# Kernel optimization log

Measured on AMD Instinct MI355X. Metric: run time of the kernel, lower is better.

The kernel has to match this reference:

```python
import jax, jax.numpy as jnp
import numpy as np

B, H, L, D = 8, 8, 512, 512
NV = 8            # n_vars
TOP_P = 0.5
ALPHA = 0.5
EPS = 1e-10


def setup_inputs() -> dict:
    key = jax.random.key(0)
    ks = jax.random.split(key, 8)
    dh = D // H
    x = jax.random.normal(ks[0], (B, L, D), jnp.float32)
    # structural masks [L, 3, L]: S (same position across vars), T (same var block), ST (rest)
    N = L // NV
    idx = jnp.arange(L)
    kk = idx[:, None]
    S = ((idx[None, :] % N == kk % N) & (idx[None, :] != kk)).astype(jnp.float32)
    T = ((idx[None, :] >= (kk // N) * N) & (idx[None, :] < (kk // N) * N + N)).astype(jnp.float32)
    ST = 1.0 - S - T
    masks = jnp.stack([S, T, ST], axis=1)  # [L, 3, L]
    s = 0.05
    W1 = jax.random.normal(ks[1], (dh, dh), jnp.float32) * s
    b1 = jnp.zeros((dh,), jnp.float32)
    W2 = jax.random.normal(ks[2], (dh, dh), jnp.float32) * s
    b2 = jnp.zeros((dh,), jnp.float32)
    Wg = jax.random.normal(ks[3], (3, L), jnp.float32) * s   # gate: Linear(L, 3, bias=False)
    Wp = jax.random.normal(ks[4], (D, D), jnp.float32) * s   # GCN proj
    bp = jnp.zeros((D,), jnp.float32)
    return {"x": x, "masks": masks, "W1": W1, "b1": b1, "W2": W2, "b2": b2,
            "Wg": Wg, "Wp": Wp, "bp": bp}


def _forward(x, masks, W1, b1, W2, b2, Wg, Wp, bp):
    Bb, Ll, Dd = x.shape
    dh = Dd // H
    xh = x.reshape(Bb, Ll, H, dh).transpose(0, 2, 1, 3)          # [B,H,L,dh]
    q = xh @ W1.T + b1
    k = xh @ W2.T + b2
    adj = jax.nn.gelu(jnp.einsum('bhid,bhjd->bhij', q, k), approximate=False)  # [B,H,L,L]
    # mask_topk: zero out the k smallest entries per row (largest=False)
    ksm = int(ALPHA * Ll)
    thr = jnp.sort(adj, axis=-1)[..., ksm - 1:ksm]               # k-th smallest value
    adj = adj * (adj > thr).astype(adj.dtype)
    # ---- mask_moe (eval mode: clean logits) ----
    xf = adj.reshape(Bb * H, Ll, Ll)
    logits = jax.nn.softmax(xf @ Wg.T, axis=-1)                  # [BH,L,3]
    loss_dyn = -(logits * jnp.log(logits + EPS)).sum(axis=1).mean()
    order = jnp.argsort(-logits, axis=-1)                        # descending
    sorted_probs = jnp.take_along_axis(logits, order, axis=-1)
    cum = jnp.cumsum(sorted_probs, axis=-1)
    m = cum > TOP_P
    thr_idx = jnp.argmax(m.astype(jnp.int32), axis=-1)           # first expert crossing top_p
    thr_mask = jax.nn.one_hot(thr_idx, 3, dtype=jnp.bool_)
    m = m & (~thr_mask)                                          # True = dropped sorted slot
    selected = (~m).astype(jnp.float32)                          # [BH,L,3] over sorted slots
    # scatter selection back to original expert order
    top_p_mask = jnp.einsum('blj,blje->ble', selected, jax.nn.one_hot(order, 3, dtype=jnp.float32))
    sp = jnp.where(m, 0.0, sorted_probs)
    imp = sp.sum(axis=0)                                         # [L,3]
    loss_imp = jnp.var(imp, ddof=1) / (jnp.mean(imp) ** 2 + EPS)
    loss = loss_imp + 0.1 * loss_dyn
    gates = top_p_mask.reshape(Bb, H, Ll, 3)
    mask = jnp.einsum('bhli,lid->bhld', gates, masks) + jnp.eye(Ll, dtype=jnp.float32)[None, None]
    adj = adj * mask
    # ---- softmax + GCN ----
    adj = jax.nn.softmax(adj, axis=-1)
    adj = adj / jnp.clip(jnp.abs(adj).sum(axis=-1, keepdims=True), 1e-12)  # F.normalize p=1
    xp = (x @ Wp.T + bp).reshape(Bb, Ll, H, dh)                  # [B,L,H,dh]
    out = jnp.einsum('bhij,bjhd->bihd', adj, xp).reshape(Bb, Ll, Dd)
    return out, loss


def reference(x, masks, W1, b1, W2, b2, Wg, Wp, bp):
    return _forward(x, masks, W1, b1, W2, b2, Wg, Wp, bp)
```

## Files before the change

### kernel.cpp

```cpp
#include <hip/hip_runtime.h>
#include <hip/hip_bf16.h>
#include <math.h>

static constexpr int kB = 8;
static constexpr int kH = 8;
static constexpr int kL = 512;
static constexpr int kD = 512;
static constexpr int kDH = 64;
static constexpr int kBH = 64;
static constexpr int kROWS = kBH * kL;

typedef short bf16x8 __attribute__((ext_vector_type(8)));
typedef float f32x4 __attribute__((ext_vector_type(4)));

__device__ __forceinline__ ushort f2bf(float f) {
    unsigned u = __float_as_uint(f);
    unsigned r = u + 0x7fffu + ((u >> 16) & 1u);
    return (ushort)(r >> 16);
}
__device__ __forceinline__ float bf2f(ushort h) {
    return __uint_as_float((unsigned)h << 16);
}
__device__ __forceinline__ unsigned mapf(float f) {
    unsigned u = __float_as_uint(f);
    return (u & 0x80000000u) ? ~u : (u | 0x80000000u);
}
__device__ __forceinline__ float unmapf(unsigned u) {
    return (u & 0x80000000u) ? __uint_as_float(u ^ 0x80000000u)
                             : __uint_as_float(~u);
}

__device__ __forceinline__ float gelu_fast(float v) {
    float z = v * 0.70710678118654752440f;
    float az = fabsf(z);
    float t = 1.0f / (1.0f + 0.3275911f * az);
    float ex = __expf(-az * az);
    float poly = t * (0.254829592f + t * (-0.284496736f + t * (1.421413741f +
                 t * (-1.453152027f + t * 1.061405429f))));
    float erfv = 1.0f - poly * ex;
    erfv = (z < 0.0f) ? -erfv : erfv;
    return 0.5f * v * (1.0f + erfv);
}

__global__ __launch_bounds__(256) void k_qk(const float* __restrict__ x,
        const float* __restrict__ W1, const float* __restrict__ b1,
        const float* __restrict__ W2, const float* __restrict__ b2,
        ushort* __restrict__ qh, ushort* __restrict__ ql,
        ushort* __restrict__ kh, ushort* __restrict__ kl) {
    int blk = blockIdx.x;
    int b = blk >> 6, h = (blk >> 3) & 7, lt = blk & 7;
    __shared__ float xt[64][68];
    __shared__ float w1t[64][68];
    __shared__ float w2t[64][68];
    int tid = threadIdx.x;
    #pragma unroll
    for (int r = 0; r < 16; ++r) {
        int e = tid + r * 256;
        int rr = e >> 6, cc = e & 63;
        xt[rr][cc]  = x[(b * kL + lt * 64 + rr) * kD + h * kDH + cc];
        w1t[rr][cc] = W1[rr * 64 + cc];
        w2t[rr][cc] = W2[rr * 64 + cc];
    }
    __syncthreads();
    int ty = tid >> 4, tx = tid & 15;
    float aq[4][4] = {}, ak[4][4] = {};
    #pragma unroll 2
    for (int c = 0; c < 64; c += 4) {
        float4 av[4], wq[4], wk[4];
        #pragma unroll
        for (int a = 0; a < 4; ++a) av[a] = *(const float4*)&xt[ty * 4 + a][c];
        #pragma unroll
        for (int j = 0; j < 4; ++j) {
            wq[j] = *(const float4*)&w1t[tx + 16 * j][c];
            wk[j] = *(const float4*)&w2t[tx + 16 * j][c];
        }
        #pragma unroll
        for (int a = 0; a < 4; ++a)
            #pragma unroll
            for (int j = 0; j < 4; ++j) {
                aq[a][j] = fmaf(av[a].x, wq[j].x, aq[a][j]);
                aq[a][j] = fmaf(av[a].y, wq[j].y, aq[a][j]);
                aq[a][j] = fmaf(av[a].z, wq[j].z, aq[a][j]);
                aq[a][j] = fmaf(av[a].w, wq[j].w, aq[a][j]);
                ak[a][j] = fmaf(av[a].x, wk[j].x, ak[a][j]);
                ak[a][j] = fmaf(av[a].y, wk[j].y, ak[a][j]);
                ak[a][j] = fmaf(av[a].z, wk[j].z, ak[a][j]);
                ak[a][j] = fmaf(av[a].w, wk[j].w, ak[a][j]);
            }
    }
    #pragma unroll
    for (int a = 0; a < 4; ++a)
        #pragma unroll
        for (int j = 0; j < 4; ++j) {
            int row = lt * 64 + ty * 4 + a;
            int col = tx + 16 * j;
            int o = ((b * kH + h) * kL + row) * kDH + col;
            float qv = aq[a][j] + b1[col];
            float kv = ak[a][j] + b2[col];
            ushort qhh = f2bf(qv), khh = f2bf(kv);
            qh[o] = qhh; ql[o] = f2bf(qv - bf2f(qhh));
            kh[o] = khh; kl[o] = f2bf(kv - bf2f(khh));
        }
}

__global__ __launch_bounds__(256) void k_adj(const ushort* __restrict__ qh,
        const ushort* __restrict__ ql, const ushort* __restrict__ kh,
        const ushort* __restrict__ kl, float* __restrict__ adj) {
    int blk = blockIdx.x;
    int bh = blk >> 6;
    int it = (blk >> 3) & 7, jt = blk & 7;
    __shared__ ushort ah[64][72], al[64][72];
    __shared__ ushort bh_[64][72], bl[64][72];
    int tid = threadIdx.x;
    int r = tid >> 2, s = tid & 3;
    size_t aoff = (size_t)(bh * kL + it * 64 + r) * kDH + s * 16;
    size_t boff = (size_t)(bh * kL + jt * 64 + r) * kDH + s * 16;
    *(int4*)&ah[r][s * 16]  = *(const int4*)&qh[aoff];
    *(int4*)&ah[r][s * 16 + 8]  = *(const int4*)&qh[aoff + 8];
    *(int4*)&al[r][s * 16]  = *(const int4*)&ql[aoff];
    *(int4*)&al[r][s * 16 + 8]  = *(const int4*)&ql[aoff + 8];
    *(int4*)&bh_[r][s * 16] = *(const int4*)&kh[boff];
    *(int4*)&bh_[r][s * 16 + 8] = *(const int4*)&kh[boff + 8];
    *(int4*)&bl[r][s * 16]  = *(const int4*)&kl[boff];
    *(int4*)&bl[r][s * 16 + 8]  = *(const int4*)&kl[boff + 8];
    __syncthreads();
    int lane = tid & 63, wave = tid >> 6;
    int wm = wave >> 1, wn = wave & 1;
    int am = wm * 32 + (lane & 15);
    int bn = wn * 32 + (lane & 15);
    int coff = (lane >> 4) * 8;
    f32x4 acc[2][2] = {};
    #pragma unroll
    for (int kk = 0; kk < 2; ++kk) {
        bf16x8 afh[2], afl[2], bfh[2], bfl[2];
        #pragma unroll
        for (int fm = 0; fm < 2; ++fm) {
            afh[fm] = *(const bf16x8*)&ah[am + fm * 16][kk * 32 + coff];
            afl[fm] = *(const bf16x8*)&al[am + fm * 16][kk * 32 + coff];
        }
        #pragma unroll
        for (int fn = 0; fn < 2; ++fn) {
            bfh[fn] = *(const bf16x8*)&bh_[bn + fn * 16][kk * 32 + coff];
            bfl[fn] = *(const bf16x8*)&bl[bn + fn * 16][kk * 32 + coff];
        }
        #pragma unroll
        for (int fm = 0; fm < 2; ++fm)
            #pragma unroll
            for (int fn = 0; fn < 2; ++fn) {
                acc[fm][fn] = __builtin_amdgcn_mfma_f32_16x16x32_bf16(
                    afh[fm], bfh[fn], acc[fm][fn], 0, 0, 0);
                acc[fm][fn] = __builtin_amdgcn_mfma_f32_16x16x32_bf16(
                    afh[fm], bfl[fn], acc[fm][fn], 0, 0, 0);
                acc[fm][fn] = __builtin_amdgcn_mfma_f32_16x16x32_bf16(
                    afl[fm], bfh[fn], acc[fm][fn], 0, 0, 0);
            }
    }
    int mrow = it * 64 + wm * 32 + (lane >> 4) * 4;
    int ncol = jt * 64 + wn * 32 + (lane & 15);
    #pragma unroll
    for (int fm = 0; fm < 2; ++fm)
        #pragma unroll
        for (int fn = 0; fn < 2; ++fn)
            #pragma unroll
            for (int rr = 0; rr < 4; ++rr)
                adj[((size_t)bh * kL + mrow + fm * 16 + rr) * kL + ncol + fn * 16] =
                    gelu_fast(acc[fm][fn][rr]);
}

__global__ __launch_bounds__(256) void k_select(const float* __restrict__ adj,
        const float* __restrict__ Wg,
        ushort* __restrict__ adjb,
        float* __restrict__ spbuf, float* __restrict__ entbuf) {
    int tid = threadIdx.x;
    int wave = tid >> 6, lane = tid & 63;
    int row = blockIdx.x * 4 + wave;
    int i = row & (kL - 1);
    const float* arow = adj + (size_t)row * kL;
    int j0 = lane * 8;

    float v[8];
    {
        float4 a0 = *(const float4*)&arow[j0];
        float4 a1 = *(const float4*)&arow[j0 + 4];
        v[0] = a0.x; v[1] = a0.y; v[2] = a0.z; v[3] = a0.w;
        v[4] = a1.x; v[5] = a1.y; v[6] = a1.z; v[7] = a1.w;
    }
    unsigned key[8];
    #pragma unroll
    for (int t = 0; t < 8; ++t) key[t] = mapf(v[t]);

    unsigned prefix = 0;
    int cbp = 0, cin = 512;
    int bit = 31;
    int mode = 0;
    while (bit >= 1) {
        unsigned qsz = 1u << (bit - 1);
        unsigned q1 = prefix + qsz;
        unsigned q2 = prefix + 2u * qsz;
        unsigned q3 = prefix + 3u * qsz;
        int c1 = 0, c2 = 0, c3 = 0;
        #pragma unroll
        for (int t = 0; t < 8; ++t) {
            c1 += (int)__popcll(__ballot(key[t] < q1));
            c2 += (int)__popcll(__ballot(key[t] < q2));
            c3 += (int)__popcll(__ballot(key[t] < q3));
        }
        if (255 < c1)      { cin = c1 - cbp; }
        else if (255 < c2) { cin = c2 - c1;  prefix = q1; cbp = c1; }
        else if (255 < c3) { cin = c3 - c2;  prefix = q2; cbp = c2; }
        else               { cin = cin - (c3 - cbp); prefix = q3; cbp = c3; }
        bit -= 2;
        int loc = 255 - cbp;
        if (cin == 1)        { mode = 2; break; }
        if (loc == 0)        { mode = 1; break; }
        if (loc == cin - 1)  { mode = 2; break; }
    }
    float thr;
    if (mode == 0) {
        thr = unmapf(prefix);
    } else {
        unsigned width = 1u << (bit + 1);
        unsigned acc = (mode == 1) ? 0xFFFFFFFFu : 0u;
        #pragma unroll
        for (int t = 0; t < 8; ++t) {
            unsigned d = key[t] - prefix;
            bool mem = d < width;
            if (mode == 1) acc = (mem && key[t] < acc) ? key[t] : acc;
            else           acc = (mem && key[t] > acc) ? key[t] : acc;
        }
        if (mode == 1) {
            #pragma unroll
            for (int off = 1; off < 64; off <<= 1)
                acc = min(acc, (unsigned)__shfl_xor((int)acc, off));
        } else {
            #pragma unroll
            for (int off = 1; off < 64; off <<= 1)
                acc = max(acc, (unsigned)__shfl_xor((int)acc, off));
        }
        thr = unmapf(acc);
    }

    union { float4 f4[2]; float f[8]; } wg0, wg1, wg2;
    wg0.f4[0] = *(const float4*)&Wg[j0];          wg0.f4[1] = *(const float4*)&Wg[j0 + 4];
    wg1.f4[0] = *(const float4*)&Wg[kL + j0];     wg1.f4[1] = *(const float4*)&Wg[kL + j0 + 4];
    wg2.f4[0] = *(const float4*)&Wg[2 * kL + j0]; wg2.f4[1] = *(const float4*)&Wg[2 * kL + j0 + 4];
    float l0 = 0.f, l1 = 0.f, l2 = 0.f;
    #pragma unroll
    for (int t = 0; t < 8; ++t) {
        float nv = (v[t] > thr) ? v[t] : 0.0f;
        v[t] = nv;
        l0 = fmaf(nv, wg0.f[t], l0);
        l1 = fmaf(nv, wg1.f[t], l1);
        l2 = fmaf(nv, wg2.f[t], l2);
    }
    #pragma unroll
    for (int off = 1; off < 64; off <<= 1) {
        l0 += __shfl_xor(l0, off);
        l1 += __shfl_xor(l1, off);
        l2 += __shfl_xor(l2, off);
    }
    float m = fmaxf(l0, fmaxf(l1, l2));
    float e0 = __expf(l0 - m), e1 = __expf(l1 - m), e2 = __expf(l2 - m);
    float s = e0 + e1 + e2;
    float p[3] = {e0 / s, e1 / s, e2 / s};
    int o0, o1, o2;
    if (p[0] >= p[1] && p[0] >= p[2]) o0 = 0;
    else if (p[1] >= p[2]) o0 = 1;
    else o0 = 2;
    int r0 = (o0 == 0) ? 1 : 0;
    int r1 = (o0 == 2) ? 1 : 2;
    if (p[r0] >= p[r1]) { o1 = r0; o2 = r1; } else { o1 = r1; o2 = r0; }
    float sp0 = p[o0], sp1 = p[o1], sp2 = p[o2];
    float c0 = sp0, c1 = sp0 + sp1, c2 = c1 + sp2;
    bool m0 = c0 > 0.5f, m1 = c1 > 0.5f, m2 = c2 > 0.5f;
    int ti = m0 ? 0 : (m1 ? 1 : 2);
    bool mm0 = m0 && (ti != 0);
    bool mm1 = m1 && (ti != 1);
    bool mm2 = m2 && (ti != 2);
    float g[3] = {0.f, 0.f, 0.f};
    g[o0] = mm0 ? 0.f : 1.f;
    g[o1] = mm1 ? 0.f : 1.f;
    g[o2] = mm2 ? 0.f : 1.f;
    if (lane == 0) {
        spbuf[row * 3 + 0] = mm0 ? 0.f : sp0;
        spbuf[row * 3 + 1] = mm1 ? 0.f : sp1;
        spbuf[row * 3 + 2] = mm2 ? 0.f : sp2;
        entbuf[row] = p[0] * __logf(p[0] + 1e-10f) +
                      p[1] * __logf(p[1] + 1e-10f) +
                      p[2] * __logf(p[2] + 1e-10f);
    }

    int i6 = i >> 6, i63 = i & 63;
    bool inb = ((lane >> 3) == i6);
    float sel1 = inb ? (g[1] + 1.0f) : g[0];
    float sel0 = inb ? g[1] : g[2];
    int lane8 = (lane & 7) * 8;
    float e[8], ls = 0.f;
    #pragma unroll
    for (int t = 0; t < 8; ++t) {
        bool ing = (lane8 + t) == i63;
        float av = v[t] * (ing ? sel1 : sel0);
        e[t] = __expf(av);
        ls += e[t];
    }
    #pragma unroll
    for (int off = 1; off < 64; off <<= 1) ls += __shfl_xor(ls, off);
    float inv = 1.0f / ls;
    union { ushort u[8]; int4 vv; } pk;
    #pragma unroll
    for (int t = 0; t < 8; ++t) pk.u[t] = f2bf(e[t] * inv);
    *(int4*)&adjb[(size_t)row * kL + j0] = pk.vv;
}

__global__ __launch_bounds__(256) void k_xp(const float* __restrict__ x,
        const float* __restrict__ Wp, const float* __restrict__ bp,
        ushort* __restrict__ xpbT) {
    int it = blockIdx.x >> 3, jt = blockIdx.x & 7;
    __shared__ ushort xbs[64][72];
    __shared__ ushort wbs[64][72];
    int tid = threadIdx.x;
    int r = tid >> 2, s = tid & 3;
    int lane = tid & 63, wave = tid >> 6;
    int wm = wave >> 1, wn = wave & 1;
    int am = wm * 32 + (lane & 15);
    int bn = wn * 32 + (lane & 15);
    int coff = (lane >> 4) * 8;
    f32x4 acc[2][2] = {};
    const float* xsrc = x + (size_t)(it * 64 + r) * kD + s * 16;
    const float* wsrc = Wp + (size_t)(jt * 64 + r) * kD + s * 16;
    for (int kt = 0; kt < 8; ++kt) {
        union { ushort u[16]; int4 v[2]; } px, pw;
        #pragma unroll
        for (int c4 = 0; c4 < 4; ++c4) {
            float4 fx = *(const float4*)(xsrc + kt * 64 + c4 * 4);
            float4 fw = *(const float4*)(wsrc + kt * 64 + c4 * 4);
            px.u[c4 * 4 + 0] = f2bf(fx.x); px.u[c4 * 4 + 1] = f2bf(fx.y);
            px.u[c4 * 4 + 2] = f2bf(fx.z); px.u[c4 * 4 + 3] = f2bf(fx.w);
            pw.u[c4 * 4 + 0] = f2bf(fw.x); pw.u[c4 * 4 + 1] = f2bf(fw.y);
            pw.u[c4 * 4 + 2] = f2bf(fw.z); pw.u[c4 * 4 + 3] = f2bf(fw.w);
        }
        __syncthreads();
        *(int4*)&xbs[r][s * 16] = px.v[0];
        *(int4*)&xbs[r][s * 16 + 8] = px.v[1];
        *(int4*)&wbs[r][s * 16] = pw.v[0];
        *(int4*)&wbs[r][s * 16 + 8] = pw.v[1];
        __syncthreads();
        #pragma unroll
        for (int kk = 0; kk < 2; ++kk) {
            bf16x8 af[2], bf[2];
            #pragma unroll
            for (int fm = 0; fm < 2; ++fm)
                af[fm] = *(const bf16x8*)&xbs[am + fm * 16][kk * 32 + coff];
            #pragma unroll
            for (int fn = 0; fn < 2; ++fn)
                bf[fn] = *(const bf16x8*)&wbs[bn + fn * 16][kk * 32 + coff];
            #pragma unroll
            for (int fm = 0; fm < 2; ++fm)
                #pragma unroll
                for (int fn = 0; fn < 2; ++fn)
                    acc[fm][fn] = __builtin_amdgcn_mfma_f32_16x16x32_bf16(
                        af[fm], bf[fn], acc[fm][fn], 0, 0, 0);
        }
    }
    #pragma unroll
    for (int fn = 0; fn < 2; ++fn) {
        int dcol = jt * 64 + wn * 32 + (lane & 15) + fn * 16;
        float bpv = bp[dcol];
        #pragma unroll
        for (int fm = 0; fm < 2; ++fm) {
            int l0 = it * 64 + wm * 32 + fm * 16 + (lane >> 4) * 4;
            union { ushort u[4]; uint2 v; } pk;
            #pragma unroll
            for (int rr = 0; rr < 4; ++rr)
                pk.u[rr] = f2bf(acc[fm][fn][rr] + bpv);
            *(uint2*)&xpbT[(size_t)dcol * (size_t)(kB * kL) + l0] = pk.v;
        }
    }
}

__global__ __launch_bounds__(256) void k_out(const ushort* __restrict__ adjb,
        const ushort* __restrict__ xpbT, float* __restrict__ out) {
    int blk = blockIdx.x;
    int bh = blk >> 3, it = blk & 7;
    int b = bh >> 3, h = bh & 7;
    __shared__ ushort as_[64][72];
    __shared__ ushort bs_[64][72];
    int tid = threadIdx.x;
    int lane = tid & 63, wave = tid >> 6;
    int wm = wave >> 1, wn = wave & 1;
    int r = tid >> 2, s = tid & 3;
    const ushort* aG = adjb + ((size_t)(bh * kL + it * 64 + r)) * kL + s * 16;
    const ushort* bG = xpbT + ((size_t)(h * kDH + r)) * (size_t)(kB * kL) + b * kL + s * 16;
    f32x4 acc[2][2] = {};
    int am = wm * 32 + (lane & 15);
    int bn = wn * 32 + (lane & 15);
    int coff = (lane >> 4) * 8;
    for (int kt = 0; kt < 8; ++kt) {
        int4 a0 = *(const int4*)(aG + kt * 64);
        int4 a1 = *(const int4*)(aG + kt * 64 + 8);
        int4 b0 = *(const int4*)(bG + kt * 64);
        int4 b1 = *(const int4*)(bG + kt * 64 + 8);
        __syncthreads();
        *(int4*)&as_[r][s * 16] = a0;
        *(int4*)&as_[r][s * 16 + 8] = a1;
        *(int4*)&bs_[r][s * 16] = b0;
        *(int4*)&bs_[r][s * 16 + 8] = b1;
        __syncthreads();
        #pragma unroll
        for (int kk = 0; kk < 2; ++kk) {
            bf16x8 af[2], bf[2];
            #pragma unroll
            for (int fm = 0; fm < 2; ++fm)
                af[fm] = *(const bf16x8*)&as_[am + fm * 16][kk * 32 + coff];
            #pragma unroll
            for (int fn = 0; fn < 2; ++fn)
                bf[fn] = *(const bf16x8*)&bs_[bn + fn * 16][kk * 32 + coff];
            #pragma unroll
            for (int fm = 0; fm < 2; ++fm)
                #pragma unroll
                for (int fn = 0; fn < 2; ++fn)
                    acc[fm][fn] = __builtin_amdgcn_mfma_f32_16x16x32_bf16(
                        af[fm], bf[fn], acc[fm][fn], 0, 0, 0);
        }
    }
    int mrow = it * 64 + wm * 32 + (lane >> 4) * 4;
    int ncol = h * kDH + wn * 32 + (lane & 15);
    #pragma unroll
    for (int fm = 0; fm < 2; ++fm)
        #pragma unroll
        for (int fn = 0; fn < 2; ++fn)
            #pragma unroll
            for (int rr = 0; rr < 4; ++rr)
                out[((size_t)b * kL + mrow + fm * 16 + rr) * kD + ncol + fn * 16] =
                    acc[fm][fn][rr];
}

__global__ __launch_bounds__(256) void k_loss1(const float* __restrict__ spbuf,
        const float* __restrict__ entbuf, float* __restrict__ imps_buf,
        float* __restrict__ entpart) {
    int tid = threadIdx.x;
    int blk = blockIdx.x;
    if (blk < 6) {
        int idx = blk * 256 + tid;
        float s = 0.f;
        for (int bh = 0; bh < kBH; ++bh)
            s += spbuf[bh * (kL * 3) + idx];
        imps_buf[idx] = s;
    } else {
        int eb = blk - 6;
        const float* src = entbuf + eb * 1024 + tid * 4;
        float4 v4 = *(const float4*)src;
        float s = v4.x + v4.y + v4.z + v4.w;
        __shared__ float red[256];
        red[tid] = s;
        __syncthreads();
        for (int st = 128; st > 0; st >>= 1) {
            if (tid < st) red[tid] += red[tid + st];
            __syncthreads();
        }
        if (tid == 0) entpart[eb] = red[0];
    }
}

__global__ __launch_bounds__(256) void k_loss2(const float* __restrict__ imps_buf,
        const float* __restrict__ entpart, float* __restrict__ out_loss) {
    __shared__ float red[256];
    int tid = threadIdx.x;
    float im[6];
    #pragma unroll
    for (int t = 0; t < 6; ++t) im[t] = imps_buf[t * 256 + tid];
    float ms = im[0] + im[1] + im[2] + im[3] + im[4] + im[5];
    red[tid] = ms;
    __syncthreads();
    for (int st = 128; st > 0; st >>= 1) {
        if (tid < st) red[tid] += red[tid + st];
        __syncthreads();
    }
    float mean = red[0] / (float)(kL * 3);
    __syncthreads();
    float vs = 0.f;
    #pragma unroll
    for (int t = 0; t < 6; ++t) { float d = im[t] - mean; vs = fmaf(d, d, vs); }
    red[tid] = vs;
    __syncthreads();
    for (int st = 128; st > 0; st >>= 1) {
        if (tid < st) red[tid] += red[tid + st];
        __syncthreads();
    }
    float var = red[0] / (float)(kL * 3 - 1);
    __syncthreads();
    red[tid] = (tid < 32) ? entpart[tid] : 0.f;
    __syncthreads();
    for (int st = 128; st > 0; st >>= 1) {
        if (tid < st) red[tid] += red[tid + st];
        __syncthreads();
    }
    if (tid == 0) {
        float loss_imp = var / (mean * mean + 1e-10f);
        float loss_dyn = -red[0] / (float)(kBH * 3);
        out_loss[0] = loss_imp + 0.1f * loss_dyn;
    }
}

extern "C" void kernel_launch(void* const* d_in, const int* in_sizes, int n_in,
                              void* d_out, int out_size, void* d_ws, size_t ws_size,
                              hipStream_t stream) {
    const float* x     = (const float*)d_in[0];
    const float* W1    = (const float*)d_in[2];
    const float* b1    = (const float*)d_in[3];
    const float* W2    = (const float*)d_in[4];
    const float* b2    = (const float*)d_in[5];
    const float* Wg    = (const float*)d_in[6];
    const float* Wp    = (const float*)d_in[7];
    const float* bp    = (const float*)d_in[8];
    float* out = (float*)d_out;
    float* ws  = (float*)d_ws;

    float*  adj    = ws;
    ushort* qh     = (ushort*)(ws + 16777216);
    ushort* ql     = (ushort*)(ws + 17825792);
    ushort* kh     = (ushort*)(ws + 18874368);
    ushort* kl     = (ushort*)(ws + 19922944);
    ushort* adjb   = (ushort*)(ws + 16777216);
    ushort* xpbT   = (ushort*)(ws + 25165824);
    float*  spbuf  = ws + 26214400;
    float*  entbuf = ws + 26312704;
    float*  imps_b = ws + 26345472;
    float*  entprt = ws + 26347008;

    k_qk<<<512, 256, 0, stream>>>(x, W1, b1, W2, b2, qh, ql, kh, kl);
    k_adj<<<kBH * 64, 256, 0, stream>>>(qh, ql, kh, kl, adj);
    k_select<<<kROWS / 4, 256, 0, stream>>>(adj, Wg, adjb, spbuf, entbuf);
    k_xp<<<512, 256, 0, stream>>>(x, Wp, bp, xpbT);
    k_out<<<512, 256, 0, stream>>>(adjb, xpbT, out);
    k_loss1<<<38, 256, 0, stream>>>(spbuf, entbuf, imps_b, entprt);
    k_loss2<<<1, 256, 0, stream>>>(imps_b, entprt, out + (size_t)kB * kL * kD);
}
```

Before: 113.3 us.

## Fuse QK^T gelu adjacency into top-k selection kernel via LDS tile

```diff
diff --git a/kernel.cpp b/kernel.cpp
--- a/kernel.cpp
+++ b/kernel.cpp
@@ -103,213 +103,199 @@
         }
 }
 
-__global__ __launch_bounds__(256) void k_adj(const ushort* __restrict__ qh,
+__global__ __launch_bounds__(256) void k_adjsel(const ushort* __restrict__ qh,
         const ushort* __restrict__ ql, const ushort* __restrict__ kh,
-        const ushort* __restrict__ kl, float* __restrict__ adj) {
-    int blk = blockIdx.x;
-    int bh = blk >> 6;
-    int it = (blk >> 3) & 7, jt = blk & 7;
-    __shared__ ushort ah[64][72], al[64][72];
-    __shared__ ushort bh_[64][72], bl[64][72];
-    int tid = threadIdx.x;
-    int r = tid >> 2, s = tid & 3;
-    size_t aoff = (size_t)(bh * kL + it * 64 + r) * kDH + s * 16;
-    size_t boff = (size_t)(bh * kL + jt * 64 + r) * kDH + s * 16;
-    *(int4*)&ah[r][s * 16]  = *(const int4*)&qh[aoff];
-    *(int4*)&ah[r][s * 16 + 8]  = *(const int4*)&qh[aoff + 8];
-    *(int4*)&al[r][s * 16]  = *(const int4*)&ql[aoff];
-    *(int4*)&al[r][s * 16 + 8]  = *(const int4*)&ql[aoff + 8];
-    *(int4*)&bh_[r][s * 16] = *(const int4*)&kh[boff];
-    *(int4*)&bh_[r][s * 16 + 8] = *(const int4*)&kh[boff + 8];
-    *(int4*)&bl[r][s * 16]  = *(const int4*)&kl[boff];
-    *(int4*)&bl[r][s * 16 + 8]  = *(const int4*)&kl[boff + 8];
-    __syncthreads();
-    int lane = tid & 63, wave = tid >> 6;
-    int wm = wave >> 1, wn = wave & 1;
-    int am = wm * 32 + (lane & 15);
-    int bn = wn * 32 + (lane & 15);
-    int coff = (lane >> 4) * 8;
-    f32x4 acc[2][2] = {};
-    #pragma unroll
-    for (int kk = 0; kk < 2; ++kk) {
-        bf16x8 afh[2], afl[2], bfh[2], bfl[2];
-        #pragma unroll
-        for (int fm = 0; fm < 2; ++fm) {
-            afh[fm] = *(const bf16x8*)&ah[am + fm * 16][kk * 32 + coff];
-            afl[fm] = *(const bf16x8*)&al[am + fm * 16][kk * 32 + coff];
-        }
-        #pragma unroll
-        for (int fn = 0; fn < 2; ++fn) {
-            bfh[fn] = *(const bf16x8*)&bh_[bn + fn * 16][kk * 32 + coff];
-            bfl[fn] = *(const bf16x8*)&bl[bn + fn * 16][kk * 32 + coff];
-        }
-        #pragma unroll
-        for (int fm = 0; fm < 2; ++fm)
-            #pragma unroll
-            for (int fn = 0; fn < 2; ++fn) {
-                acc[fm][fn] = __builtin_amdgcn_mfma_f32_16x16x32_bf16(
-                    afh[fm], bfh[fn], acc[fm][fn], 0, 0, 0);
-                acc[fm][fn] = __builtin_amdgcn_mfma_f32_16x16x32_bf16(
-                    afh[fm], bfl[fn], acc[fm][fn], 0, 0, 0);
-                acc[fm][fn] = __builtin_amdgcn_mfma_f32_16x16x32_bf16(
-                    afl[fm], bfh[fn], acc[fm][fn], 0, 0, 0);
-            }
-    }
-    int mrow = it * 64 + wm * 32 + (lane >> 4) * 4;
-    int ncol = jt * 64 + wn * 32 + (lane & 15);
-    #pragma unroll
-    for (int fm = 0; fm < 2; ++fm)
-        #pragma unroll
-        for (int fn = 0; fn < 2; ++fn)
-            #pragma unroll
-            for (int rr = 0; rr < 4; ++rr)
-                adj[((size_t)bh * kL + mrow + fm * 16 + rr) * kL + ncol + fn * 16] =
-                    gelu_fast(acc[fm][fn][rr]);
-}
-
-__global__ __launch_bounds__(256) void k_select(const float* __restrict__ adj,
-        const float* __restrict__ Wg,
+        const ushort* __restrict__ kl, const float* __restrict__ Wg,
         ushort* __restrict__ adjb,
         float* __restrict__ spbuf, float* __restrict__ entbuf) {
+    __shared__ ushort qhs[16][72], qls[16][72];
+    __shared__ ushort khs[64][72], kls[64][72];
+    __shared__ float adjt[16][516];
     int tid = threadIdx.x;
-    int wave = tid >> 6, lane = tid & 63;
-    int row = blockIdx.x * 4 + wave;
-    int i = row & (kL - 1);
-    const float* arow = adj + (size_t)row * kL;
-    int j0 = lane * 8;
-
-    float v[8];
+    int blk = blockIdx.x;
+    int bh = blk >> 5, rt = blk & 31;
+    int lane = tid & 63, wv = tid >> 6;
+
     {
-        float4 a0 = *(const float4*)&arow[j0];
-        float4 a1 = *(const float4*)&arow[j0 + 4];
-        v[0] = a0.x; v[1] = a0.y; v[2] = a0.z; v[3] = a0.w;
-        v[4] = a1.x; v[5] = a1.y; v[6] = a1.z; v[7] = a1.w;
-    }
-    unsigned key[8];
-    #pragma unroll
-    for (int t = 0; t < 8; ++t) key[t] = mapf(v[t]);
-
-    unsigned prefix = 0;
-    int cbp = 0, cin = 512;
-    int bit = 31;
-    int mode = 0;
-    while (bit >= 1) {
-        unsigned qsz = 1u << (bit - 1);
-        unsigned q1 = prefix + qsz;
-        unsigned q2 = prefix + 2u * qsz;
-        unsigned q3 = prefix + 3u * qsz;
-        int c1 = 0, c2 = 0, c3 = 0;
+        int row = tid >> 4, col = (tid & 15) * 4;
+        size_t off = (size_t)(bh * kL + rt * 16 + row) * kDH + col;
+        *(uint2*)&qhs[row][col] = *(const uint2*)&qh[off];
+        *(uint2*)&qls[row][col] = *(const uint2*)&ql[off];
+    }
+
+    int coff = (lane >> 4) * 8;
+    int arow = lane & 15;
+    int brow = wv * 16 + (lane & 15);
+    int rs = tid >> 2, ss = tid & 3;
+    f32x4 acc[8] = {};
+    #pragma unroll
+    for (int jt = 0; jt < 8; ++jt) {
+        __syncthreads();
+        size_t boff = (size_t)(bh * kL + jt * 64 + rs) * kDH + ss * 16;
+        *(int4*)&khs[rs][ss * 16]     = *(const int4*)&kh[boff];
+        *(int4*)&khs[rs][ss * 16 + 8] = *(const int4*)&kh[boff + 8];
+        *(int4*)&kls[rs][ss * 16]     = *(const int4*)&kl[boff];
+        *(int4*)&kls[rs][ss * 16 + 8] = *(const int4*)&kl[boff + 8];
+        __syncthreads();
+        #pragma unroll
+        for (int kk = 0; kk < 2; ++kk) {
+            bf16x8 ah8 = *(const bf16x8*)&qhs[arow][kk * 32 + coff];
+            bf16x8 al8 = *(const bf16x8*)&qls[arow][kk * 32 + coff];
+            bf16x8 bh8 = *(const bf16x8*)&khs[brow][kk * 32 + coff];
+            bf16x8 bl8 = *(const bf16x8*)&kls[brow][kk * 32 + coff];
+            acc[jt] = __builtin_amdgcn_mfma_f32_16x16x32_bf16(ah8, bh8, acc[jt], 0, 0, 0);
+            acc[jt] = __builtin_amdgcn_mfma_f32_16x16x32_bf16(ah8, bl8, acc[jt], 0, 0, 0);
+            acc[jt] = __builtin_amdgcn_mfma_f32_16x16x32_bf16(al8, bh8, acc[jt], 0, 0, 0);
+        }
+    }
+    __syncthreads();
+    #pragma unroll
+    for (int m = 0; m < 8; ++m) {
+        int col = wv * 16 + m * 64 + (lane & 15);
+        #pragma unroll
+        for (int rr = 0; rr < 4; ++rr) {
+            int row = (lane >> 4) * 4 + rr;
+            adjt[row][col] = gelu_fast(acc[m][rr]);
+        }
+    }
+    __syncthreads();
+
+    float wgA[8], wgB[8], wgC[8];
+    #pragma unroll
+    for (int t = 0; t < 8; ++t) {
+        wgA[t] = Wg[t * 64 + lane];
+        wgB[t] = Wg[kL + t * 64 + lane];
+        wgC[t] = Wg[2 * kL + t * 64 + lane];
+    }
+
+    for (int rsel = 0; rsel < 4; ++rsel) {
+        int rl = wv * 4 + rsel;
+        int i = rt * 16 + rl;
+        int rowg = bh * kL + i;
+        float v[8];
+        unsigned key[8];
         #pragma unroll
         for (int t = 0; t < 8; ++t) {
-            c1 += (int)__popcll(__ballot(key[t] < q1));
-            c2 += (int)__popcll(__ballot(key[t] < q2));
-            c3 += (int)__popcll(__ballot(key[t] < q3));
-        }
-        if (255 < c1)      { cin = c1 - cbp; }
-        else if (255 < c2) { cin = c2 - c1;  prefix = q1; cbp = c1; }
-        else if (255 < c3) { cin = c3 - c2;  prefix = q2; cbp = c2; }
-        else               { cin = cin - (c3 - cbp); prefix = q3; cbp = c3; }
-        bit -= 2;
-        int loc = 255 - cbp;
-        if (cin == 1)        { mode = 2; break; }
-        if (loc == 0)        { mode = 1; break; }
-        if (loc == cin - 1)  { mode = 2; break; }
-    }
-    float thr;
-    if (mode == 0) {
-        thr = unmapf(prefix);
-    } else {
-        unsigned width = 1u << (bit + 1);
-        unsigned acc = (mode == 1) ? 0xFFFFFFFFu : 0u;
+            v[t] = adjt[rl][t * 64 + lane];
+            key[t] = mapf(v[t]);
+        }
+
+        unsigned prefix = 0;
+        int cbp = 0, cin = 512;
+        int bit = 31;
+        int mode = 0;
+        while (bit >= 1) {
+            unsigned qsz = 1u << (bit - 1);
+            unsigned q1 = prefix + qsz;
+            unsigned q2 = prefix + 2u * qsz;
+            unsigned q3 = prefix + 3u * qsz;
+            int c1 = 0, c2 = 0, c3 = 0;
+            #pragma unroll
+            for (int t = 0; t < 8; ++t) {
+                c1 += (int)__popcll(__ballot(key[t] < q1));
+                c2 += (int)__popcll(__ballot(key[t] < q2));
+                c3 += (int)__popcll(__ballot(key[t] < q3));
+            }
+            if (255 < c1)      { cin = c1 - cbp; }
+            else if (255 < c2) { cin = c2 - c1;  prefix = q1; cbp = c1; }
+            else if (255 < c3) { cin = c3 - c2;  prefix = q2; cbp = c2; }
+            else               { cin = cin - (c3 - cbp); prefix = q3; cbp = c3; }
+            bit -= 2;
+            int loc = 255 - cbp;
+            if (cin == 1)        { mode = 2; break; }
+            if (loc == 0)        { mode = 1; break; }
+            if (loc == cin - 1)  { mode = 2; break; }
+        }
+        float thr;
+        if (mode == 0) {
+            thr = unmapf(prefix);
+        } else {
+            unsigned width = 1u << (bit + 1);
+            unsigned accu = (mode == 1) ? 0xFFFFFFFFu : 0u;
+            #pragma unroll
+            for (int t = 0; t < 8; ++t) {
+                unsigned d = key[t] - prefix;
+                bool mem = d < width;
+                if (mode == 1) accu = (mem && key[t] < accu) ? key[t] : accu;
+                else           accu = (mem && key[t] > accu) ? key[t] : accu;
+            }
+            if (mode == 1) {
+                #pragma unroll
+                for (int off = 1; off < 64; off <<= 1)
+                    accu = min(accu, (unsigned)__shfl_xor((int)accu, off));
+            } else {
+                #pragma unroll
+                for (int off = 1; off < 64; off <<= 1)
+                    accu = max(accu, (unsigned)__shfl_xor((int)accu, off));
+            }
+            thr = unmapf(accu);
+        }
+
+        float l0 = 0.f, l1 = 0.f, l2 = 0.f;
         #pragma unroll
         for (int t = 0; t < 8; ++t) {
-            unsigned d = key[t] - prefix;
-            bool mem = d < width;
-            if (mode == 1) acc = (mem && key[t] < acc) ? key[t] : acc;
-            else           acc = (mem && key[t] > acc) ? key[t] : acc;
-        }
-        if (mode == 1) {
-            #pragma unroll
-            for (int off = 1; off < 64; off <<= 1)
-                acc = min(acc, (unsigned)__shfl_xor((int)acc, off));
-        } else {
-            #pragma unroll
-            for (int off = 1; off < 64; off <<= 1)
-                acc = max(acc, (unsigned)__shfl_xor((int)acc, off));
-        }
-        thr = unmapf(acc);
-    }
-
-    union { float4 f4[2]; float f[8]; } wg0, wg1, wg2;
-    wg0.f4[0] = *(const float4*)&Wg[j0];          wg0.f4[1] = *(const float4*)&Wg[j0 + 4];
-    wg1.f4[0] = *(const float4*)&Wg[kL + j0];     wg1.f4[1] = *(const float4*)&Wg[kL + j0 + 4];
-    wg2.f4[0] = *(const float4*)&Wg[2 * kL + j0]; wg2.f4[1] = *(const float4*)&Wg[2 * kL + j0 + 4];
-    float l0 = 0.f, l1 = 0.f, l2 = 0.f;
-    #pragma unroll
-    for (int t = 0; t < 8; ++t) {
-        float nv = (v[t] > thr) ? v[t] : 0.0f;
-        v[t] = nv;
-        l0 = fmaf(nv, wg0.f[t], l0);
-        l1 = fmaf(nv, wg1.f[t], l1);
-        l2 = fmaf(nv, wg2.f[t], l2);
-    }
-    #pragma unroll
-    for (int off = 1; off < 64; off <<= 1) {
-        l0 += __shfl_xor(l0, off);
-        l1 += __shfl_xor(l1, off);
-        l2 += __shfl_xor(l2, off);
-    }
-    float m = fmaxf(l0, fmaxf(l1, l2));
-    float e0 = __expf(l0 - m), e1 = __expf(l1 - m), e2 = __expf(l2 - m);
-    float s = e0 + e1 + e2;
-    float p[3] = {e0 / s, e1 / s, e2 / s};
-    int o0, o1, o2;
-    if (p[0] >= p[1] && p[0] >= p[2]) o0 = 0;
-    else if (p[1] >= p[2]) o0 = 1;
-    else o0 = 2;
-    int r0 = (o0 == 0) ? 1 : 0;
-    int r1 = (o0 == 2) ? 1 : 2;
-    if (p[r0] >= p[r1]) { o1 = r0; o2 = r1; } else { o1 = r1; o2 = r0; }
-    float sp0 = p[o0], sp1 = p[o1], sp2 = p[o2];
-    float c0 = sp0, c1 = sp0 + sp1, c2 = c1 + sp2;
-    bool m0 = c0 > 0.5f, m1 = c1 > 0.5f, m2 = c2 > 0.5f;
-    int ti = m0 ? 0 : (m1 ? 1 : 2);
-    bool mm0 = m0 && (ti != 0);
-    bool mm1 = m1 && (ti != 1);
-    bool mm2 = m2 && (ti != 2);
-    float g[3] = {0.f, 0.f, 0.f};
-    g[o0] = mm0 ? 0.f : 1.f;
-    g[o1] = mm1 ? 0.f : 1.f;
-    g[o2] = mm2 ? 0.f : 1.f;
-    if (lane == 0) {
-        spbuf[row * 3 + 0] = mm0 ? 0.f : sp0;
-        spbuf[row * 3 + 1] = mm1 ? 0.f : sp1;
-        spbuf[row * 3 + 2] = mm2 ? 0.f : sp2;
-        entbuf[row] = p[0] * __logf(p[0] + 1e-10f) +
-                      p[1] * __logf(p[1] + 1e-10f) +
-                      p[2] * __logf(p[2] + 1e-10f);
-    }
-
-    int i6 = i >> 6, i63 = i & 63;
-    bool inb = ((lane >> 3) == i6);
-    float sel1 = inb ? (g[1] + 1.0f) : g[0];
-    float sel0 = inb ? g[1] : g[2];
-    int lane8 = (lane & 7) * 8;
-    float e[8], ls = 0.f;
-    #pragma unroll
-    for (int t = 0; t < 8; ++t) {
-        bool ing = (lane8 + t) == i63;
-        float av = v[t] * (ing ? sel1 : sel0);
-        e[t] = __expf(av);
-        ls += e[t];
-    }
-    #pragma unroll
-    for (int off = 1; off < 64; off <<= 1) ls += __shfl_xor(ls, off);
-    float inv = 1.0f / ls;
-    union { ushort u[8]; int4 vv; } pk;
-    #pragma unroll
-    for (int t = 0; t < 8; ++t) pk.u[t] = f2bf(e[t] * inv);
-    *(int4*)&adjb[(size_t)row * kL + j0] = pk.vv;
+            float nv = (v[t] > thr) ? v[t] : 0.0f;
+            v[t] = nv;
+            l0 = fmaf(nv, wgA[t], l0);
+            l1 = fmaf(nv, wgB[t], l1);
+            l2 = fmaf(nv, wgC[t], l2);
+        }
+        #pragma unroll
+        for (int off = 1; off < 64; off <<= 1) {
+            l0 += __shfl_xor(l0, off);
+            l1 += __shfl_xor(l1, off);
+            l2 += __shfl_xor(l2, off);
+        }
+        float m = fmaxf(l0, fmaxf(l1, l2));
+        float e0 = __expf(l0 - m), e1 = __expf(l1 - m), e2 = __expf(l2 - m);
+        float s = e0 + e1 + e2;
+        float p[3] = {e0 / s, e1 / s, e2 / s};
+        int o0, o1, o2;
+        if (p[0] >= p[1] && p[0] >= p[2]) o0 = 0;
+        else if (p[1] >= p[2]) o0 = 1;
+        else o0 = 2;
+        int r0 = (o0 == 0) ? 1 : 0;
+        int r1 = (o0 == 2) ? 1 : 2;
+        if (p[r0] >= p[r1]) { o1 = r0; o2 = r1; } else { o1 = r1; o2 = r0; }
+        float sp0 = p[o0], sp1 = p[o1], sp2 = p[o2];
+        float c0 = sp0, c1 = sp0 + sp1, c2 = c1 + sp2;
+        bool m0 = c0 > 0.5f, m1 = c1 > 0.5f, m2 = c2 > 0.5f;
+        int ti = m0 ? 0 : (m1 ? 1 : 2);
+        bool mm0 = m0 && (ti != 0);
+        bool mm1 = m1 && (ti != 1);
+        bool mm2 = m2 && (ti != 2);
+        float g[3] = {0.f, 0.f, 0.f};
+        g[o0] = mm0 ? 0.f : 1.f;
+        g[o1] = mm1 ? 0.f : 1.f;
+        g[o2] = mm2 ? 0.f : 1.f;
+        if (lane == 0) {
+            spbuf[rowg * 3 + 0] = mm0 ? 0.f : sp0;
+            spbuf[rowg * 3 + 1] = mm1 ? 0.f : sp1;
+            spbuf[rowg * 3 + 2] = mm2 ? 0.f : sp2;
+            entbuf[rowg] = p[0] * __logf(p[0] + 1e-10f) +
+                           p[1] * __logf(p[1] + 1e-10f) +
+                           p[2] * __logf(p[2] + 1e-10f);
+        }
+
+        int i6 = i >> 6, i63 = i & 63;
+        bool ing = (lane == i63);
+        float selT = ing ? (g[1] + 1.0f) : g[1];
+        float selO = ing ? g[0] : g[2];
+        float e[8], ls = 0.f;
+        #pragma unroll
+        for (int t = 0; t < 8; ++t) {
+            float mm = (t == i6) ? selT : selO;
+            float av = v[t] * mm;
+            e[t] = __expf(av);
+            ls += e[t];
+        }
+        #pragma unroll
+        for (int off = 1; off < 64; off <<= 1) ls += __shfl_xor(ls, off);
+        float inv = 1.0f / ls;
+        #pragma unroll
+        for (int t = 0; t < 8; ++t)
+            adjb[(size_t)rowg * kL + t * 64 + lane] = f2bf(e[t] * inv);
+    }
 }
 
 __global__ __launch_bounds__(256) void k_xp(const float* __restrict__ x,
@@ -516,21 +502,19 @@
     float* out = (float*)d_out;
     float* ws  = (float*)d_ws;
 
-    float*  adj    = ws;
-    ushort* qh     = (ushort*)(ws + 16777216);
-    ushort* ql     = (ushort*)(ws + 17825792);
-    ushort* kh     = (ushort*)(ws + 18874368);
-    ushort* kl     = (ushort*)(ws + 19922944);
-    ushort* adjb   = (ushort*)(ws + 16777216);
-    ushort* xpbT   = (ushort*)(ws + 25165824);
-    float*  spbuf  = ws + 26214400;
-    float*  entbuf = ws + 26312704;
-    float*  imps_b = ws + 26345472;
-    float*  entprt = ws + 26347008;
+    ushort* qh     = (ushort*)(ws);
+    ushort* ql     = (ushort*)(ws + 1048576);
+    ushort* kh     = (ushort*)(ws + 2097152);
+    ushort* kl     = (ushort*)(ws + 3145728);
+    ushort* adjb   = (ushort*)(ws + 4194304);
+    ushort* xpbT   = (ushort*)(ws + 12582912);
+    float*  spbuf  = ws + 13631488;
+    float*  entbuf = ws + 13729792;
+    float*  imps_b = ws + 13762560;
+    float*  entprt = ws + 13764096;
 
     k_qk<<<512, 256, 0, stream>>>(x, W1, b1, W2, b2, qh, ql, kh, kl);
-    k_adj<<<kBH * 64, 256, 0, stream>>>(qh, ql, kh, kl, adj);
-    k_select<<<kROWS / 4, 256, 0, stream>>>(adj, Wg, adjb, spbuf, entbuf);
+    k_adjsel<<<kBH * 32, 256, 0, stream>>>(qh, ql, kh, kl, Wg, adjb, spbuf, entbuf);
     k_xp<<<512, 256, 0, stream>>>(x, Wp, bp, xpbT);
     k_out<<<512, 256, 0, stream>>>(adjb, xpbT, out);
     k_loss1<<<38, 256, 0, stream>>>(spbuf, entbuf, imps_b, entprt);
```

Result: slower. 144.3 us (+27.4%).
